# Kernel tuning notes

Hardware: AMD Instinct MI355X
Metric: run time of the kernel (lower is better)

## Reference

```python
import jax, jax.numpy as jnp
import numpy as np


def chamfer_bidirectional(p1, p2):
    """p1: [B,N,3], p2: [B,M,3]. Returns (min_sq_dist1 [B,N], min_sq_dist2 [B,M])."""
    # squared pairwise distances via ||a||^2 + ||b||^2 - 2 a.b  (avoids [B,N,M,3] diff tensor)
    n1 = jnp.sum(p1 * p1, axis=-1)          # [B,N]
    n2 = jnp.sum(p2 * p2, axis=-1)          # [B,M]
    cross = jnp.einsum('bnd,bmd->bnm', p1, p2)  # [B,N,M]
    d = n1[:, :, None] + n2[:, None, :] - 2.0 * cross  # [B,N,M]
    d = jnp.maximum(d, 0.0)
    return jnp.min(d, axis=2), jnp.min(d, axis=1)


def setup_inputs() -> dict:
    key = jax.random.key(0)
    k1, k2, k3, k4, k5 = jax.random.split(key, 5)
    B = 8
    return {
        'pred': jax.random.normal(k1, (B, 10, 3), dtype=jnp.float32),
        'target': jax.random.normal(k2, (B, 10, 3), dtype=jnp.float32),
        'coarse': jax.random.normal(k3, (B, 3, 1024), dtype=jnp.float32),
        'fine': jax.random.normal(k4, (B, 3, 4096), dtype=jnp.float32),
        'gt_pc': jax.random.normal(k5, (B, 4096, 3), dtype=jnp.float32),
    }


def reference(pred, target, coarse, fine, gt_pc):
    kp_loss = jnp.mean((pred - target) ** 2)
    c1, c2 = chamfer_bidirectional(jnp.transpose(coarse, (0, 2, 1)), gt_pc)
    f1, f2 = chamfer_bidirectional(jnp.transpose(fine, (0, 2, 1)), gt_pc)
    coarse_loss = jnp.mean(c1) + jnp.mean(c2)
    fine_loss = jnp.mean(f1) + jnp.mean(f2)
    return kp_loss + coarse_loss + fine_loss
```

## Files before the change

### kernel.cpp

```cpp
#include <hip/hip_runtime.h>
#include <math.h>

typedef __attribute__((ext_vector_type(8))) short bf16x8;
typedef __attribute__((ext_vector_type(4))) float f32x4;
typedef __attribute__((ext_vector_type(4))) unsigned int uint4v;

#define ROWMIN_OFF 256
#define N_ROWMIN   106496
#define FRAG0      458752
#define SZ_FINE    (8*256*1024)
#define SZ_COARSE  (8*64*1024)
#define OFF_FINEA  ((size_t)FRAG0)
#define OFF_FINEB  ((size_t)FRAG0 + SZ_FINE)
#define OFF_GTA    ((size_t)FRAG0 + 2*(size_t)SZ_FINE)
#define OFF_GTB    ((size_t)FRAG0 + 3*(size_t)SZ_FINE)
#define OFF_COARA  ((size_t)FRAG0 + 4*(size_t)SZ_FINE)
#define OFF_COARB  ((size_t)FRAG0 + 4*(size_t)SZ_FINE + SZ_COARSE)
#define WS_NEED    ((size_t)FRAG0 + 4*(size_t)SZ_FINE + 2*(size_t)SZ_COARSE)

__device__ __forceinline__ unsigned short bf16_rn(float f) {
    unsigned u = __float_as_uint(f);
    u += 0x7FFFu + ((u >> 16) & 1u);
    return (unsigned short)(u >> 16);
}
__device__ __forceinline__ float bf16_f(unsigned short h) {
    return __uint_as_float(((unsigned)h) << 16);
}

__global__ __launch_bounds__(256) void prebuild(
    const float* __restrict__ fine, const float* __restrict__ gt,
    const float* __restrict__ coarse, unsigned* __restrict__ wsu)
{
    const int id = blockIdx.x * 256 + threadIdx.x;
    const int FRAGU = 8 * 1152 * 64;
    char* wsc = (char*)wsu;
    if (id < FRAGU) {
        const int lane = id & 63;
        int t = (id >> 6) % 1152;
        const int b = (id >> 6) / 1152;
        const int role = (t >= 576) ? 1 : 0;
        if (role) t -= 576;
        float x, y, z; size_t outoff;
        if (t < 256) {
            const float* p = fine + (size_t)b * 3 * 4096;
            int pt = t * 16 + (lane & 15);
            x = p[pt]; y = p[4096 + pt]; z = p[8192 + pt];
            outoff = (role ? OFF_FINEB : OFF_FINEA) + ((size_t)(b * 256 + t) * 64 + lane) * 16;
        } else if (t < 512) {
            int tile = t - 256;
            const float* p = gt + (size_t)b * 4096 * 3;
            int pt = tile * 16 + (lane & 15);
            x = p[3 * pt]; y = p[3 * pt + 1]; z = p[3 * pt + 2];
            outoff = (role ? OFF_GTB : OFF_GTA) + ((size_t)(b * 256 + tile) * 64 + lane) * 16;
        } else {
            int tile = t - 512;
            const float* p = coarse + (size_t)b * 3 * 1024;
            int pt = tile * 16 + (lane & 15);
            x = p[pt]; y = p[1024 + pt]; z = p[2048 + pt];
            outoff = (role ? OFF_COARB : OFF_COARA) + ((size_t)(b * 64 + tile) * 64 + lane) * 16;
        }
        const int kw = lane >> 4;
        unsigned short hx = bf16_rn(x), hy = bf16_rn(y), hz = bf16_rn(z);
        float fx = bf16_f(hx), fy = bf16_f(hy), fz = bf16_f(hz);
        unsigned short lx = bf16_rn(x - fx), ly = bf16_rn(y - fy), lz = bf16_rn(z - fz);
        float n = fmaf(x, x, fmaf(y, y, z * z));
        unsigned short nh = bf16_rn(n);
        unsigned short nl = bf16_rn(n - bf16_f(nh));
        const unsigned short one = 0x3F80;
        unsigned short e0=0,e1=0,e2=0,e3=0,e4=0,e5=0,e6=0,e7=0;
        if (kw < 2) {
            if (!role) {
                unsigned short t0 = bf16_rn(-2.f * fx), t1 = bf16_rn(-2.f * fy), t2 = bf16_rn(-2.f * fz);
                unsigned short u0 = bf16_rn(-2.f * bf16_f(lx)), u1 = bf16_rn(-2.f * bf16_f(ly)), u2 = bf16_rn(-2.f * bf16_f(lz));
                if (kw == 0) { e0=t0; e1=t1; e2=t2; e3=t0; e4=t1; e5=t2; e6=u0; e7=u1; }
                else         { e0=u2; e1=one; e2=one; e3=nh; e4=nl; }
            } else {
                if (kw == 0) { e0=hx; e1=hy; e2=hz; e3=lx; e4=ly; e5=lz; e6=hx; e7=hy; }
                else         { e0=hz; e1=nh; e2=nl; e3=one; e4=one; }
            }
        }
        uint4v v = { (unsigned)e0 | ((unsigned)e1 << 16),
                     (unsigned)e2 | ((unsigned)e3 << 16),
                     (unsigned)e4 | ((unsigned)e5 << 16),
                     (unsigned)e6 | ((unsigned)e7 << 16) };
        *(uint4v*)(wsc + outoff) = v;
    } else if (id < FRAGU + N_ROWMIN) {
        ((unsigned*)(wsc + ROWMIN_OFF))[id - FRAGU] = 0x7F800000u;
    } else if (id == FRAGU + N_ROWMIN) {
        wsu[0] = 0u;
        wsu[1] = 0u;
    }
}

__global__ __launch_bounds__(256, 4) void chamfer_mfma(unsigned char* __restrict__ wsb)
{
    const int w    = blockIdx.x * 4 + (threadIdx.x >> 6);
    const int lane = threadIdx.x & 63;

    int b, octet, ms, TA, TB, rowbase, rowsb;
    size_t Aoff, Boff;
    if (w < 2048)      { int u = w;        b = u >> 8; int r = u & 255; octet = r >> 3; ms = r & 7;
                         Aoff = OFF_FINEA; TA = 256; Boff = OFF_GTB;   TB = 256; rowbase = 0;     rowsb = 4096; }
    else if (w < 4096) { int u = w - 2048; b = u >> 8; int r = u & 255; octet = r >> 3; ms = r & 7;
                         Aoff = OFF_GTA;   TA = 256; Boff = OFF_FINEB; TB = 256; rowbase = 32768; rowsb = 4096; }
    else if (w < 4608) { int u = w - 4096; b = u >> 6; int r = u & 63;  octet = r >> 3; ms = r & 7;
                         Aoff = OFF_COARA; TA = 64;  Boff = OFF_GTB;   TB = 256; rowbase = 65536; rowsb = 1024; }
    else               { int u = w - 4608; b = u >> 6; int r = u & 63;  octet = r >> 1; ms = r & 1;
                         Aoff = OFF_GTA;   TA = 256; Boff = OFF_COARB; TB = 64;  rowbase = 73728; rowsb = 4096; }

    bf16x8 af[8];
#pragma unroll
    for (int s = 0; s < 8; ++s)
        af[s] = *(const bf16x8*)(wsb + Aoff + ((size_t)((b * TA + octet * 8 + s) * 64 + lane)) * 16);

    const unsigned char* bp = wsb + Boff + ((size_t)((b * TB + ms * 32) * 64 + lane)) * 16;

    float rm[8][4];
#pragma unroll
    for (int s = 0; s < 8; ++s) { rm[s][0]=rm[s][1]=rm[s][2]=rm[s][3]=3.402823466e38f; }

    const f32x4 zero = {0.f, 0.f, 0.f, 0.f};
#pragma unroll 2
    for (int mt = 0; mt < 32; ++mt) {
        bf16x8 bf = *(const bf16x8*)(bp + (size_t)mt * 1024);
#pragma unroll
        for (int s = 0; s < 8; ++s) {
            f32x4 r = __builtin_amdgcn_mfma_f32_16x16x32_bf16(af[s], bf, zero, 0, 0, 0);
            rm[s][0] = fminf(rm[s][0], r[0]);
            rm[s][1] = fminf(rm[s][1], r[1]);
            rm[s][2] = fminf(rm[s][2], r[2]);
            rm[s][3] = fminf(rm[s][3], r[3]);
        }
    }

    unsigned* rowmin = (unsigned*)(wsb + ROWMIN_OFF);
    const int rg = rowbase + b * rowsb + octet * 128;
#pragma unroll
    for (int s = 0; s < 8; ++s)
#pragma unroll
        for (int j = 0; j < 4; ++j) {
            float v = fmaxf(rm[s][j], 0.f);
            v = fminf(v, __shfl_xor(v, 1, 64));
            v = fminf(v, __shfl_xor(v, 2, 64));
            v = fminf(v, __shfl_xor(v, 4, 64));
            v = fminf(v, __shfl_xor(v, 8, 64));
            if ((lane & 15) == 0)
                atomicMin(rowmin + rg + s * 16 + (lane >> 4) * 4 + j, __float_as_uint(v));
        }
}

__global__ __launch_bounds__(256) void reduce_all(
    unsigned* __restrict__ wsu,
    const float* __restrict__ pred, const float* __restrict__ target,
    float* __restrict__ out)
{
    const unsigned* rowmin = (const unsigned*)((const char*)wsu + ROWMIN_OFF);
    const int tid = threadIdx.x;
    float s = 0.f;
    for (int i = blockIdx.x * 256 + tid; i < N_ROWMIN; i += gridDim.x * 256) {
        float v = __uint_as_float(rowmin[i]);
        float sc = (i >= 65536 && i < 73728) ? (1.f / 8192.f) : (1.f / 32768.f);
        s = fmaf(v, sc, s);
    }
    if (blockIdx.x == 0 && tid < 240) {
        float d = pred[tid] - target[tid];
        s = fmaf(d, d * (1.f / 240.f), s);
    }
    for (int off = 32; off > 0; off >>= 1) s += __shfl_down(s, off, 64);
    __shared__ float r4[4];
    if ((tid & 63) == 0) r4[tid >> 6] = s;
    __syncthreads();
    if (tid == 0) {
        atomicAdd((float*)wsu, r4[0] + r4[1] + r4[2] + r4[3]);
        __threadfence();
        unsigned old = atomicAdd(wsu + 1, 1u);
        if (old == gridDim.x - 1) {
            __threadfence();
            out[0] = atomicAdd((float*)wsu, 0.f);
        }
    }
}

#define SBMAX 2112
template<int CHUNK, bool A_PLANAR, bool B_PLANAR>
__device__ __forceinline__ float chamfer_block(
    const float* __restrict__ A, int An, const float* __restrict__ B, int Bn,
    int lbid, float scale, float (&sb)[4][SBMAX], float (&red)[512])
{
    constexpr int NSEG = 16;
    constexpr int SEG  = CHUNK / NSEG;
    constexpr int LOG_SEG = (CHUNK == 2048) ? 7 : 6;
    constexpr int SEGP = SEG + 4;
    const int bpb = An >> 5, batch = lbid / bpb, ablk = lbid % bpb;
    const float* __restrict__ Ab = A + (size_t)batch * 3 * An;
    const float* __restrict__ Bb = B + (size_t)batch * 3 * Bn;
    const int tid = threadIdx.x, slot = tid & 15, sp = tid >> 4;
    const int p0 = ablk * 32 + slot, p1 = p0 + 16;
    float a0x, a0y, a0z, a1x, a1y, a1z;
    if (A_PLANAR) { a0x=Ab[p0]; a0y=Ab[An+p0]; a0z=Ab[2*An+p0]; a1x=Ab[p1]; a1y=Ab[An+p1]; a1z=Ab[2*An+p1]; }
    else { a0x=Ab[3*p0]; a0y=Ab[3*p0+1]; a0z=Ab[3*p0+2]; a1x=Ab[3*p1]; a1y=Ab[3*p1+1]; a1z=Ab[3*p1+2]; }
    const float a0s = fmaf(a0x,a0x,fmaf(a0y,a0y,a0z*a0z));
    const float a1s = fmaf(a1x,a1x,fmaf(a1y,a1y,a1z*a1z));
    const float BIG = 3.402823466e38f;
    float n00=BIG,n01=BIG,n10=BIG,n11=BIG;
    for (int t0 = 0; t0 < Bn; t0 += CHUNK) {
#pragma unroll
        for (int i = 0; i < CHUNK / 256; ++i) {
            const int k = tid + i * 256; float x, y, z;
            if (B_PLANAR) { x=Bb[t0+k]; y=Bb[Bn+t0+k]; z=Bb[2*Bn+t0+k]; }
            else { int base = 3*(t0+k); x=Bb[base]; y=Bb[base+1]; z=Bb[base+2]; }
            const int addr = (k >> LOG_SEG) * SEGP + (k & (SEG - 1));
            sb[0][addr]=-2.f*x; sb[1][addr]=-2.f*y; sb[2][addr]=-2.f*z; sb[3][addr]=fmaf(x,x,fmaf(y,y,z*z));
        }
        __syncthreads();
        const float4* px = (const float4*)&sb[0][sp*SEGP];
        const float4* py = (const float4*)&sb[1][sp*SEGP];
        const float4* pz = (const float4*)&sb[2][sp*SEGP];
        const float4* pw = (const float4*)&sb[3][sp*SEGP];
#pragma unroll 2
        for (int g = 0; g < SEG / 4; ++g) {
            float4 x=px[g], y=py[g], z=pz[g], w=pw[g];
            float d0,d1,d2,d3;
            d0=fmaf(a0x,x.x,fmaf(a0y,y.x,fmaf(a0z,z.x,w.x)));
            d1=fmaf(a0x,x.y,fmaf(a0y,y.y,fmaf(a0z,z.y,w.y)));
            d2=fmaf(a0x,x.z,fmaf(a0y,y.z,fmaf(a0z,z.z,w.z)));
            d3=fmaf(a0x,x.w,fmaf(a0y,y.w,fmaf(a0z,z.w,w.w)));
            n00=fminf(fminf(d0,d1),n00); n01=fminf(fminf(d2,d3),n01);
            d0=fmaf(a1x,x.x,fmaf(a1y,y.x,fmaf(a1z,z.x,w.x)));
            d1=fmaf(a1x,x.y,fmaf(a1y,y.y,fmaf(a1z,z.y,w.y)));
            d2=fmaf(a1x,x.z,fmaf(a1y,y.z,fmaf(a1z,z.z,w.z)));
            d3=fmaf(a1x,x.w,fmaf(a1y,y.w,fmaf(a1z,z.w,w.w)));
            n10=fminf(fminf(d0,d1),n10); n11=fminf(fminf(d2,d3),n11);
        }
        __syncthreads();
    }
    red[sp*16+slot]=fminf(n00,n01); red[256+sp*16+slot]=fminf(n10,n11);
    __syncthreads();
#pragma unroll
    for (int st = 8; st > 0; st >>= 1) {
        if (sp < st) {
            red[sp*16+slot]=fminf(red[sp*16+slot],red[(sp+st)*16+slot]);
            red[256+sp*16+slot]=fminf(red[256+sp*16+slot],red[256+(sp+st)*16+slot]);
        }
        __syncthreads();
    }
    float contrib = 0.f;
    if (tid < 16) {
        float d = fmaxf(0.f,a0s+red[slot]) + fmaxf(0.f,a1s+red[256+slot]);
        d *= scale;
#pragma unroll
        for (int off = 8; off > 0; off >>= 1) d += __shfl_down(d, off, 16);
        contrib = d;
    }
    return contrib;
}

__device__ __forceinline__ float kp_block(const float* __restrict__ a,
                                          const float* __restrict__ b, int n, float (&red)[512])
{
    int tid = threadIdx.x; float s = 0.f;
    for (int i = tid; i < n; i += 256) { float d = a[i]-b[i]; s = fmaf(d,d,s); }
    for (int off = 32; off > 0; off >>= 1) s += __shfl_down(s, off, 64);
    if ((tid & 63) == 0) red[tid >> 6] = s;
    __syncthreads();
    float r = 0.f;
    if (tid == 0) r = (red[0]+red[1]+red[2]+red[3]) / (float)n;
    return r;
}

__global__ __launch_bounds__(256, 4) void fused_all(
    const float* __restrict__ pred, const float* __restrict__ target, int nkp,
    const float* __restrict__ coarse, int Nc, const float* __restrict__ fine, int Nf,
    const float* __restrict__ gt, int M, int r1, int r2, int r3, int r4,
    float sc_f1, float sc_f2, float sc_c1, float sc_c2, float* __restrict__ ws)
{
    __shared__ __align__(16) float sb[4][SBMAX];
    __shared__ float red[512];
    const int bid = blockIdx.x;
    float contrib;
    if (bid < r1)      contrib = chamfer_block<2048,true, false>(fine,  Nf, gt,     M,  bid,      sc_f1, sb, red);
    else if (bid < r2) contrib = chamfer_block<2048,false,true >(gt,    M,  fine,   Nf, bid - r1, sc_f2, sb, red);
    else if (bid < r3) contrib = chamfer_block<2048,true, false>(coarse,Nc, gt,     M,  bid - r2, sc_c1, sb, red);
    else if (bid < r4) contrib = chamfer_block<1024,false,true >(gt,    M,  coarse, Nc, bid - r3, sc_c2, sb, red);
    else               contrib = kp_block(pred, target, nkp, red);
    if (threadIdx.x == 0) ws[bid] = contrib;
}

__global__ __launch_bounds__(256) void finalize(const float* __restrict__ ws, int n,
                                                float* __restrict__ out)
{
    int tid = threadIdx.x; float s = 0.f;
    for (int i = tid; i < n; i += 256) s += ws[i];
    for (int off = 32; off > 0; off >>= 1) s += __shfl_down(s, off, 64);
    __shared__ float r[4];
    if ((tid & 63) == 0) r[tid >> 6] = s;
    __syncthreads();
    if (tid == 0) out[0] = r[0] + r[1] + r[2] + r[3];
}

extern "C" void kernel_launch(void* const* d_in, const int* in_sizes, int n_in,
                              void* d_out, int out_size, void* d_ws, size_t ws_size,
                              hipStream_t stream) {
    const float* pred   = (const float*)d_in[0];
    const float* target = (const float*)d_in[1];
    const float* coarse = (const float*)d_in[2];
    const float* fine   = (const float*)d_in[3];
    const float* gt     = (const float*)d_in[4];
    float* out = (float*)d_out;

    const int nkp = in_sizes[0];
    const int B   = nkp / 30;
    const int Nc  = in_sizes[2] / (3 * B);
    const int Nf  = in_sizes[3] / (3 * B);
    const int M   = in_sizes[4] / (3 * B);

    const bool mfma_ok = (B == 8 && Nc == 1024 && Nf == 4096 && M == 4096 &&
                          ws_size >= WS_NEED);
    if (mfma_ok) {
        unsigned* wsu = (unsigned*)d_ws;
        const int FRAGU = 8 * 1152 * 64;
        const int pre_total = FRAGU + N_ROWMIN + 1;
        prebuild<<<(pre_total + 255) / 256, 256, 0, stream>>>(fine, gt, coarse, wsu);
        chamfer_mfma<<<1280, 256, 0, stream>>>((unsigned char*)d_ws);
        reduce_all<<<120, 256, 0, stream>>>(wsu, pred, target, out);
    } else {
        float* ws = (float*)d_ws;
        const int r1 = B * (Nf / 32);
        const int r2 = r1 + B * (M / 32);
        const int r3 = r2 + B * (Nc / 32);
        const int r4 = r3 + B * (M / 32);
        const int nb = r4 + 1;
        fused_all<<<nb, 256, 0, stream>>>(
            pred, target, nkp, coarse, Nc, fine, Nf, gt, M,
            r1, r2, r3, r4,
            1.0f / (B * Nf), 1.0f / (B * M), 1.0f / (B * Nc), 1.0f / (B * M), ws);
        finalize<<<1, 256, 0, stream>>>(ws, nb, out);
    }
}
```

Before: 99.18 us.

## Stage B fragments in LDS, double per-wave row tiles, replace atomicMin with partial planes

Each block now loads its 32 B-tiles into shared memory once, and its four waves read them from there instead of each wave reading global memory. Each wave holds 16 A-fragments instead of 8, so every B load feeds twice as many MFMAs and the grid halves to 640 blocks. Per-row atomicMin into a pre-initialised buffer is replaced by plain stores into separate partial planes indexed by the ms slice. The reduce kernel then takes the min across planes and clamps at zero. This removes the atomic traffic and the init pass, but raises register pressure (launch bounds drop from 4 to 3 blocks) and makes the reduce read more data.

After: 240.3 us. 2.42x slower.

```diff
diff --git a/kernel.cpp b/kernel.cpp
--- a/kernel.cpp
+++ b/kernel.cpp
@@ -5,18 +5,22 @@
 typedef __attribute__((ext_vector_type(4))) float f32x4;
 typedef __attribute__((ext_vector_type(4))) unsigned int uint4v;
 
-#define ROWMIN_OFF 256
-#define N_ROWMIN   106496
-#define FRAG0      458752
-#define SZ_FINE    (8*256*1024)
-#define SZ_COARSE  (8*64*1024)
-#define OFF_FINEA  ((size_t)FRAG0)
-#define OFF_FINEB  ((size_t)FRAG0 + SZ_FINE)
-#define OFF_GTA    ((size_t)FRAG0 + 2*(size_t)SZ_FINE)
-#define OFF_GTB    ((size_t)FRAG0 + 3*(size_t)SZ_FINE)
-#define OFF_COARA  ((size_t)FRAG0 + 4*(size_t)SZ_FINE)
-#define OFF_COARB  ((size_t)FRAG0 + 4*(size_t)SZ_FINE + SZ_COARSE)
-#define WS_NEED    ((size_t)FRAG0 + 4*(size_t)SZ_FINE + 2*(size_t)SZ_COARSE)
+#define BO    64
+#define P_F1  0
+#define P_F2  262144
+#define P_C1  524288
+#define P_C2  589824
+#define N_ROWS 106496
+#define FRAG0     ((size_t)4 << 20)
+#define SZ_FINE   (8*256*1024)
+#define SZ_COARSE (8*64*1024)
+#define OFF_FINEA (FRAG0)
+#define OFF_FINEB (OFF_FINEA + SZ_FINE)
+#define OFF_GTA   (OFF_FINEB + SZ_FINE)
+#define OFF_GTB   (OFF_GTA + SZ_FINE)
+#define OFF_COARA (OFF_GTB + SZ_FINE)
+#define OFF_COARB (OFF_COARA + SZ_COARSE)
+#define WS_NEED   (OFF_COARB + SZ_COARSE)
 
 __device__ __forceinline__ unsigned short bf16_rn(float f) {
     unsigned u = __float_as_uint(f);
@@ -84,47 +88,54 @@
                      (unsigned)e4 | ((unsigned)e5 << 16),
                      (unsigned)e6 | ((unsigned)e7 << 16) };
         *(uint4v*)(wsc + outoff) = v;
-    } else if (id < FRAGU + N_ROWMIN) {
-        ((unsigned*)(wsc + ROWMIN_OFF))[id - FRAGU] = 0x7F800000u;
-    } else if (id == FRAGU + N_ROWMIN) {
+    } else if (id == FRAGU) {
         wsu[0] = 0u;
         wsu[1] = 0u;
     }
 }
 
-__global__ __launch_bounds__(256, 4) void chamfer_mfma(unsigned char* __restrict__ wsb)
-{
-    const int w    = blockIdx.x * 4 + (threadIdx.x >> 6);
-    const int lane = threadIdx.x & 63;
-
-    int b, octet, ms, TA, TB, rowbase, rowsb;
+__global__ __launch_bounds__(256, 3) void chamfer_mfma(unsigned char* __restrict__ wsb)
+{
+    __shared__ float4 sb4[2048];
+    const int bid  = blockIdx.x;
+    const int tid  = threadIdx.x;
+    const int w    = tid >> 6;
+    const int lane = tid & 63;
+
+    int b, rgq, ms, TA, TB, pbase, plane, rowsB;
     size_t Aoff, Boff;
-    if (w < 2048)      { int u = w;        b = u >> 8; int r = u & 255; octet = r >> 3; ms = r & 7;
-                         Aoff = OFF_FINEA; TA = 256; Boff = OFF_GTB;   TB = 256; rowbase = 0;     rowsb = 4096; }
-    else if (w < 4096) { int u = w - 2048; b = u >> 8; int r = u & 255; octet = r >> 3; ms = r & 7;
-                         Aoff = OFF_GTA;   TA = 256; Boff = OFF_FINEB; TB = 256; rowbase = 32768; rowsb = 4096; }
-    else if (w < 4608) { int u = w - 4096; b = u >> 6; int r = u & 63;  octet = r >> 3; ms = r & 7;
-                         Aoff = OFF_COARA; TA = 64;  Boff = OFF_GTB;   TB = 256; rowbase = 65536; rowsb = 1024; }
-    else               { int u = w - 4608; b = u >> 6; int r = u & 63;  octet = r >> 1; ms = r & 1;
-                         Aoff = OFF_GTA;   TA = 256; Boff = OFF_COARB; TB = 64;  rowbase = 73728; rowsb = 4096; }
-
-    bf16x8 af[8];
-#pragma unroll
-    for (int s = 0; s < 8; ++s)
-        af[s] = *(const bf16x8*)(wsb + Aoff + ((size_t)((b * TA + octet * 8 + s) * 64 + lane)) * 16);
-
-    const unsigned char* bp = wsb + Boff + ((size_t)((b * TB + ms * 32) * 64 + lane)) * 16;
-
-    float rm[8][4];
-#pragma unroll
-    for (int s = 0; s < 8; ++s) { rm[s][0]=rm[s][1]=rm[s][2]=rm[s][3]=3.402823466e38f; }
-
+    if (bid < 256)      { int u = bid;       b=u>>5; int r=u&31; rgq=r>>3; ms=r&7;
+                          Aoff=OFF_FINEA; TA=256; Boff=OFF_GTB;   TB=256; pbase=P_F1; plane=32768; rowsB=4096; }
+    else if (bid < 512) { int u = bid - 256; b=u>>5; int r=u&31; rgq=r>>3; ms=r&7;
+                          Aoff=OFF_GTA;   TA=256; Boff=OFF_FINEB; TB=256; pbase=P_F2; plane=32768; rowsB=4096; }
+    else if (bid < 576) { int u = bid - 512; b=u>>3; ms=u&7; rgq=0;
+                          Aoff=OFF_COARA; TA=64;  Boff=OFF_GTB;   TB=256; pbase=P_C1; plane=8192;  rowsB=1024; }
+    else                { int u = bid - 576; b=u>>3; int r=u&7; rgq=r>>1; ms=r&1;
+                          Aoff=OFF_GTA;   TA=256; Boff=OFF_COARB; TB=64;  pbase=P_C2; plane=32768; rowsB=4096; }
+
+    const int rowgrp = rgq * 4 + w;
+
+    const float4* __restrict__ src = (const float4*)(wsb + Boff + (size_t)(b * TB + ms * 32) * 1024);
+#pragma unroll
+    for (int i = 0; i < 8; ++i) sb4[tid + i * 256] = src[tid + i * 256];
+    __syncthreads();
+
+    bf16x8 af[16];
+    const unsigned char* ap = wsb + Aoff + ((size_t)((b * TA + rowgrp * 16) * 64 + lane)) * 16;
+#pragma unroll
+    for (int s = 0; s < 16; ++s) af[s] = *(const bf16x8*)(ap + (size_t)s * 1024);
+
+    float rm[16][4];
+#pragma unroll
+    for (int s = 0; s < 16; ++s) { rm[s][0]=rm[s][1]=rm[s][2]=rm[s][3]=3.402823466e38f; }
+
+    const bf16x8* __restrict__ sbf = (const bf16x8*)sb4;
     const f32x4 zero = {0.f, 0.f, 0.f, 0.f};
 #pragma unroll 2
     for (int mt = 0; mt < 32; ++mt) {
-        bf16x8 bf = *(const bf16x8*)(bp + (size_t)mt * 1024);
-#pragma unroll
-        for (int s = 0; s < 8; ++s) {
+        bf16x8 bf = sbf[mt * 64 + lane];
+#pragma unroll
+        for (int s = 0; s < 16; ++s) {
             f32x4 r = __builtin_amdgcn_mfma_f32_16x16x32_bf16(af[s], bf, zero, 0, 0, 0);
             rm[s][0] = fminf(rm[s][0], r[0]);
             rm[s][1] = fminf(rm[s][1], r[1]);
@@ -133,19 +144,21 @@
         }
     }
 
-    unsigned* rowmin = (unsigned*)(wsb + ROWMIN_OFF);
-    const int rg = rowbase + b * rowsb + octet * 128;
-#pragma unroll
-    for (int s = 0; s < 8; ++s)
+    float* part = (float*)wsb;
+    const int rbase = b * rowsB + rowgrp * 256;
+#pragma unroll
+    for (int s = 0; s < 16; ++s)
 #pragma unroll
         for (int j = 0; j < 4; ++j) {
-            float v = fmaxf(rm[s][j], 0.f);
+            float v = rm[s][j];
             v = fminf(v, __shfl_xor(v, 1, 64));
             v = fminf(v, __shfl_xor(v, 2, 64));
             v = fminf(v, __shfl_xor(v, 4, 64));
             v = fminf(v, __shfl_xor(v, 8, 64));
-            if ((lane & 15) == 0)
-                atomicMin(rowmin + rg + s * 16 + (lane >> 4) * 4 + j, __float_as_uint(v));
+            if ((lane & 15) == 0) {
+                int row = rbase + s * 16 + (lane >> 4) * 4 + j;
+                part[BO + pbase + ms * plane + row] = v;
+            }
         }
 }
 
@@ -154,13 +167,18 @@
     const float* __restrict__ pred, const float* __restrict__ target,
     float* __restrict__ out)
 {
-    const unsigned* rowmin = (const unsigned*)((const char*)wsu + ROWMIN_OFF);
+    const float* part = (const float*)wsu;
     const int tid = threadIdx.x;
     float s = 0.f;
-    for (int i = blockIdx.x * 256 + tid; i < N_ROWMIN; i += gridDim.x * 256) {
-        float v = __uint_as_float(rowmin[i]);
-        float sc = (i >= 65536 && i < 73728) ? (1.f / 8192.f) : (1.f / 32768.f);
-        s = fmaf(v, sc, s);
+    for (int i = blockIdx.x * 256 + tid; i < N_ROWS; i += gridDim.x * 256) {
+        int r = i, off, np, plane; float sc;
+        if (r < 32768)      { off = P_F1; np = 8; plane = 32768; sc = 1.f / 32768.f; }
+        else if (r < 65536) { r -= 32768; off = P_F2; np = 8; plane = 32768; sc = 1.f / 32768.f; }
+        else if (r < 73728) { r -= 65536; off = P_C1; np = 8; plane = 8192;  sc = 1.f / 8192.f; }
+        else                { r -= 73728; off = P_C2; np = 2; plane = 32768; sc = 1.f / 32768.f; }
+        float m = part[BO + off + r];
+        for (int p = 1; p < np; ++p) m = fminf(m, part[BO + off + p * plane + r]);
+        s = fmaf(fmaxf(m, 0.f), sc, s);
     }
     if (blockIdx.x == 0 && tid < 240) {
         float d = pred[tid] - target[tid];
@@ -319,9 +337,8 @@
     if (mfma_ok) {
         unsigned* wsu = (unsigned*)d_ws;
         const int FRAGU = 8 * 1152 * 64;
-        const int pre_total = FRAGU + N_ROWMIN + 1;
-        prebuild<<<(pre_total + 255) / 256, 256, 0, stream>>>(fine, gt, coarse, wsu);
-        chamfer_mfma<<<1280, 256, 0, stream>>>((unsigned char*)d_ws);
+        prebuild<<<(FRAGU + 1 + 255) / 256, 256, 0, stream>>>(fine, gt, coarse, wsu);
+        chamfer_mfma<<<640, 256, 0, stream>>>((unsigned char*)d_ws);
         reduce_all<<<120, 256, 0, stream>>>(wsu, pred, target, out);
     } else {
         float* ws = (float*)d_ws;
```
